# Performance work log

Measured on AMD Instinct MI355X. Metric: run time of the kernel, lower is better.

Reference implementation:

```python
import math
import jax
import jax.numpy as jnp
import numpy as np

B = 2; Hrv = 16; Wrv = 1024; Crv = 64; Cb = 128; Cout = 128
D = 128; K = 5; NH = 8; NP = 4; DH = D // NH
Hbev = 220; Wbev = 220
RMAX = 55.0; XMIN = -55.0; XMAX = 55.0; YMIN = -55.0; YMAX = 55.0
EDGE_GAIN = 4.0; KLW = 1e-4

ELEV = np.array([-30.67, -29.33, -28.0, -26.66, -25.33, -24.0, -22.67, -21.33, -20.0, -18.67, -17.33, -16.0, -14.67, -13.33, -12.0, -10.67, -9.33, -8.0, -6.66, -5.33, -4.0, -2.67, -1.33, 0.0, 1.33, 2.67, 4.0, 5.33, 6.67, 8.0, 9.33, 10.67], dtype=np.float32)


def _buffers():
    groups = ELEV[::-1].reshape(Hrv, 32 // Hrv)
    steps = np.deg2rad(groups.max(1) - groups.min(1)).astype(np.float32)
    # torch Tensor.repeat == tile (faithful to original, even though rows end up interleaved)
    elev_steps = np.tile(steps, Wrv).reshape(Hrv, Wrv)
    means = np.deg2rad(groups.mean(1)).astype(np.float32)
    elevation = np.repeat(means, Wrv).reshape(Hrv, Wrv)  # numpy repeat == elementwise
    az_line = np.linspace(-np.pi, np.pi, Wrv + 1, dtype=np.float64)[:-1]
    az_step = float(az_line[1] - az_line[0])
    az_line = (az_line + az_step / 2).astype(np.float32)
    azimuth = np.broadcast_to(az_line[None, :], (Hrv, Wrv)).astype(np.float32).copy()
    offsets = np.linspace(-0.6, 0.6, K).astype(np.float32)
    u_vec = np.stack([np.cos(elevation) * np.cos(azimuth), np.cos(elevation) * np.sin(azimuth), np.sin(elevation)], 0).astype(np.float32)
    return (jnp.asarray(elev_steps), jnp.asarray(elevation), jnp.asarray(azimuth), az_step, jnp.asarray(offsets), jnp.asarray(u_vec))


def conv1x1(x, w, b):
    return jnp.einsum('bchw,oc->bohw', x, w) + b[None, :, None, None]


def groupnorm(x, g, gamma, beta, eps=1e-5):
    b_, c, h, w = x.shape
    xr = x.reshape(b_, g, c // g, h, w)
    m = xr.mean(axis=(2, 3, 4), keepdims=True)
    v = xr.var(axis=(2, 3, 4), keepdims=True)
    xn = ((xr - m) * jax.lax.rsqrt(v + eps)).reshape(b_, c, h, w)
    return xn * gamma[None, :, None, None] + beta[None, :, None, None]


def bilinear_sample(v_t, loc, H, W):
    # v_t: [B,NH,H*W,DH]; loc: [B,Nq,NH,NP,2] in [0,1]; grid_sample align_corners=False, zeros pad
    x = loc[..., 0] * W - 0.5
    y = loc[..., 1] * H - 0.5
    x0 = jnp.floor(x); y0 = jnp.floor(y)
    wx = x - x0; wy = y - y0
    x0i = x0.astype(jnp.int32); y0i = y0.astype(jnp.int32)
    b_, n_, nh_, p_ = x.shape

    def gather(xi, yi):
        valid = (xi >= 0) & (xi < W) & (yi >= 0) & (yi < H)
        idx = jnp.clip(yi, 0, H - 1) * W + jnp.clip(xi, 0, W - 1)
        idx_t = idx.transpose(0, 2, 1, 3).reshape(b_, nh_, n_ * p_)
        g = jnp.take_along_axis(v_t, idx_t[..., None], axis=2).reshape(b_, nh_, n_, p_, -1)
        return g * valid.transpose(0, 2, 1, 3)[..., None]

    wxt = wx.transpose(0, 2, 1, 3)[..., None]
    wyt = wy.transpose(0, 2, 1, 3)[..., None]
    g = gather(x0i, y0i) * (1 - wxt) * (1 - wyt)
    g = g + gather(x0i + 1, y0i) * wxt * (1 - wyt)
    g = g + gather(x0i, y0i + 1) * (1 - wxt) * wyt
    g = g + gather(x0i + 1, y0i + 1) * wxt * wyt
    return g  # [B,NH,Nq,NP,DH]


def setup_inputs():
    key = jax.random.key(0)
    ks = jax.random.split(key, 20)
    def rn(k, shape, s=0.02):
        return jax.random.normal(k, shape, jnp.float32) * s
    inp = {}
    inp['x_rv'] = jax.random.normal(ks[0], (B, Hrv, Wrv, Crv), jnp.float32)
    inp['bev'] = jax.random.normal(ks[1], (B, Cb, Hbev, Wbev), jnp.float32)
    inp['lidar2ego_mat'] = jnp.eye(4, dtype=jnp.float32)[None] + 0.01 * jax.random.normal(ks[2], (1, 4, 4), jnp.float32)
    inp['w_q'] = rn(ks[3], (D, Crv)); inp['b_q'] = jnp.zeros((D,), jnp.float32)
    inp['w_v'] = rn(ks[4], (D, Cb)); inp['b_v'] = jnp.zeros((D,), jnp.float32)
    inp['w_o'] = rn(ks[5], (Cout, D)); inp['b_o'] = jnp.zeros((Cout,), jnp.float32)
    inp['qs_w1'] = rn(ks[6], (D, D + 6)); inp['qs_b1'] = jnp.zeros((D,), jnp.float32)
    inp['qs_w2'] = rn(ks[7], (D, D)); inp['qs_b2'] = jnp.zeros((D,), jnp.float32)
    inp['rh_w1'] = rn(ks[8], (128, Crv + 3)); inp['rh_b1'] = jnp.zeros((128,), jnp.float32)
    inp['rh_g1'] = jnp.ones((128,), jnp.float32); inp['rh_bt1'] = jnp.zeros((128,), jnp.float32)
    inp['rh_w2'] = rn(ks[9], (64, 128, 3, 3))
    inp['rh_g2'] = jnp.ones((64,), jnp.float32); inp['rh_bt2'] = jnp.zeros((64,), jnp.float32)
    inp['rh_w3'] = rn(ks[10], (4, 64)); inp['rh_b3'] = jnp.zeros((4,), jnp.float32)
    inp['off_w'] = rn(ks[11], (NH * K * NP * 2, D)); inp['off_b'] = rn(ks[12], (NH * K * NP * 2,), 0.5)
    inp['aw_w'] = rn(ks[13], (NH * K * NP, D)); inp['aw_b'] = jnp.zeros((NH * K * NP,), jnp.float32)
    inp['val_w'] = rn(ks[14], (D, D)); inp['val_b'] = jnp.zeros((D,), jnp.float32)
    inp['out_w'] = rn(ks[15], (D, D)); inp['out_b'] = jnp.zeros((D,), jnp.float32)
    return inp


def reference(x_rv, bev, lidar2ego_mat, w_q, b_q, w_v, b_v, w_o, b_o, qs_w1, qs_b1, qs_w2, qs_b2, rh_w1, rh_b1, rh_g1, rh_bt1, rh_w2, rh_g2, rh_bt2, rh_w3, rh_b3, off_w, off_b, aw_w, aw_b, val_w, val_b, out_w, out_b):
    elev_steps, elevation, azimuth, az_step, offsets, u_vec = _buffers()
    x = jnp.transpose(x_rv, (0, 3, 1, 2))  # [B,Crv,Hrv,Wrv]
    Q0 = conv1x1(x, w_q, b_q)
    Vmap = conv1x1(bev, w_v, b_v)
    range_in = jnp.concatenate([x, jnp.broadcast_to(u_vec[None], (B, 3, Hrv, Wrv))], axis=1)
    h = jax.nn.gelu(groupnorm(conv1x1(range_in, rh_w1, rh_b1), 8, rh_g1, rh_bt1), approximate=False)
    hp = jnp.pad(h, ((0, 0), (0, 0), (1, 1), (1, 1)), mode='wrap')  # circular padding
    h = jax.lax.conv_general_dilated(hp, rh_w2, (1, 1), 'VALID', dimension_numbers=('NCHW', 'OIHW', 'NCHW'))
    h = jax.nn.gelu(groupnorm(h, 8, rh_g2, rh_bt2), approximate=False)
    head = conv1x1(h, rh_w3, rh_b3)  # [B,4,Hrv,Wrv]
    mu = jax.nn.sigmoid(head[:, 0:1]) * RMAX
    sd = jax.nn.softplus(head[:, 1:2]) + 1e-3
    se = jax.nn.sigmoid(head[:, 2:3]) * elev_steps + 1e-3
    sa = jax.nn.sigmoid(head[:, 3:4]) * az_step + 1e-3
    depth = mu[:, 0][..., None] + sd[:, 0][..., None] * offsets  # [B,Hrv,Wrv,K]
    elevs = elevation[None, :, :, None] + se[:, 0][..., None] * offsets
    azs = azimuth[None, :, :, None] + sa[:, 0][..., None] * offsets
    ce = jnp.cos(elevs)
    x_l = depth * ce * jnp.cos(azs)
    y_l = depth * ce * jnp.sin(azs)
    z_l = depth * jnp.sin(elevs)
    NK = Hrv * Wrv * K
    p = jnp.stack([x_l.reshape(B, NK), y_l.reshape(B, NK), z_l.reshape(B, NK), jnp.ones((B, NK), x_l.dtype)], axis=-1)
    p_ego = jnp.matmul(p, lidar2ego_mat)  # [B,NK,4]
    rx = jax.nn.sigmoid(EDGE_GAIN * ((p_ego[..., 0] - XMIN) / (XMAX - XMIN) - 0.5))
    ry = jax.nn.sigmoid(EDGE_GAIN * ((p_ego[..., 1] - YMIN) / (YMAX - YMIN) - 0.5))
    ref = jnp.stack([rx, ry], axis=-1).reshape(B, Hrv * Wrv, K, 2)
    sig_feat = jnp.concatenate([sd, se, sa, 1.0 / (sd + 1e-6), 1.0 / (se + 1e-6), 1.0 / (sa + 1e-6)], axis=1)
    Q = conv1x1(jax.nn.gelu(conv1x1(jnp.concatenate([Q0, sig_feat], axis=1), qs_w1, qs_b1), approximate=False), qs_w2, qs_b2)
    query = jnp.transpose(Q, (0, 2, 3, 1)).reshape(B, Hrv * Wrv, D)
    value = jnp.transpose(Vmap.reshape(B, D, Hbev * Wbev), (0, 2, 1))  # [B,HW,D]
    # MSDA -- all K levels share the same BEV value map (value was repeat(1,K,1))
    v = (value @ val_w.T + val_b).reshape(B, Hbev * Wbev, NH, DH)
    v_t = jnp.transpose(v, (0, 2, 1, 3))  # [B,NH,HW,DH]
    Nq = Hrv * Wrv
    smp_off = (query @ off_w.T + off_b).reshape(B, Nq, NH, K, NP, 2)
    attn = jax.nn.softmax((query @ aw_w.T + aw_b).reshape(B, Nq, NH, K * NP), axis=-1).reshape(B, Nq, NH, K, NP)
    norm = jnp.array([Wbev, Hbev], jnp.float32)
    loc = ref[:, :, None, :, None, :] + smp_off / norm  # [B,Nq,NH,K,NP,2]
    out = jnp.zeros((B, Nq, NH, DH), jnp.float32)
    for l in range(K):
        smp = bilinear_sample(v_t, loc[:, :, :, l], Hbev, Wbev)
        out = out + jnp.einsum('bhnpd,bnhp->bnhd', smp, attn[:, :, :, l])
    y_msda = out.reshape(B, Nq, D) @ out_w.T + out_b + query  # mmcv identity residual
    y = jnp.transpose(y_msda.reshape(B, Hrv, Wrv, D), (0, 3, 1, 2))
    y = conv1x1(y, w_o, b_o)
    mu_norm = mu / RMAX
    sr = jnp.maximum(sd, 1e-6)
    saz = sa / az_step
    sel = se / elev_steps
    L_kl = 0.5 * (mu_norm ** 2 + sr ** 2 - jnp.log(sr ** 2) - 1.0) \
         + 0.5 * (saz ** 2 - jnp.log(saz ** 2) - 1.0) \
         + 0.5 * (sel ** 2 - jnp.log(sel ** 2) - 1.0)
    kl = KLW * L_kl.mean()
    y = y.reshape(B, Hrv, Wrv, -1)  # faithful to torch .view on NCHW (no permute)
    return (y, kl)
```

## Files before the change

### kernel.cpp

```cpp
#include <hip/hip_runtime.h>
#include <math.h>

#define HRV 16
#define WRV 1024
#define NPIX 16384
#define NBEV 48400
#define BSZ 2

typedef __attribute__((ext_vector_type(8))) short short8;
typedef __attribute__((ext_vector_type(4))) float f32x4;

struct RVConsts {
  float steps[16];
  float means[16];
  float az_step_f;
  float pad_;
  double step_d;
  double az0;
  double az_half;
};

__device__ __forceinline__ float geluf(float x) {
  return 0.5f * x * (1.0f + erff(x * 0.70710678118654752440f));
}
__device__ __forceinline__ float sigmoidf_(float x) {
  return 1.0f / (1.0f + expf(-x));
}
__device__ __forceinline__ float softplusf_(float x) {
  return fmaxf(x, 0.0f) + log1pf(expf(-fabsf(x)));
}
__device__ __forceinline__ float azimf(int w, double step_d, double az0, double az_half) {
  double az = (double)w * step_d + az0;
  az += az_half;
  return (float)az;
}
__device__ __forceinline__ unsigned short f2bf(float f) {
  unsigned int u = __builtin_bit_cast(unsigned int, f);
  u = u + 0x7FFFu + ((u >> 16) & 1u);
  return (unsigned short)(u >> 16);
}
__device__ __forceinline__ float bf2f(unsigned short h) {
  unsigned int u = ((unsigned int)h) << 16;
  return __builtin_bit_cast(float, u);
}

__global__ __launch_bounds__(256) void k_rh1_q0(
    const float* __restrict__ x_rv,
    const unsigned short* __restrict__ rhW1p, const float* __restrict__ rh_b1,
    const unsigned short* __restrict__ wqp, const float* __restrict__ b_q,
    float* __restrict__ t1, unsigned short* __restrict__ q0,
    float* __restrict__ sums1, RVConsts C) {
  __shared__ unsigned short xin[64][104];
  __shared__ float wred[4][8][2];
  int b = blockIdx.y;
  int n0 = blockIdx.x * 64;
  int tid = threadIdx.x;
  const float* src = x_rv + ((size_t)b * NPIX + n0) * 64;
  for (int i = tid; i < 1024; i += 256) {
    int p = i >> 4, c = (i & 15) * 4;
    float4 v4 = *(const float4*)(src + p * 64 + c);
    xin[p][c] = f2bf(v4.x);
    xin[p][c + 1] = f2bf(v4.y);
    xin[p][c + 2] = f2bf(v4.z);
    xin[p][c + 3] = f2bf(v4.w);
  }
  if (tid < 64) {
    int n = n0 + tid;
    int h = n >> 10, w = n & 1023;
    float E = C.means[h];
    float A = azimf(w, C.step_d, C.az0, C.az_half);
    float ce = cosf(E);
    xin[tid][64] = f2bf(ce * cosf(A));
    xin[tid][65] = f2bf(ce * sinf(A));
    xin[tid][66] = f2bf(sinf(E));
    for (int c = 67; c < 104; c++) xin[tid][c] = 0;
  }
  __syncthreads();
  int wave = tid >> 6, l = tid & 63;
  int lr = l & 15, lk = l >> 4;
  f32x4 acc[8], accq[8];
#pragma unroll
  for (int nt = 0; nt < 8; nt++) {
    float b1 = rh_b1[nt * 16 + lr], b2 = b_q[nt * 16 + lr];
    acc[nt] = (f32x4){b1, b1, b1, b1};
    accq[nt] = (f32x4){b2, b2, b2, b2};
  }
#pragma unroll
  for (int ks = 0; ks < 3; ks++) {
    short8 a = *(const short8*)&xin[wave * 16 + lr][ks * 32 + lk * 8];
#pragma unroll
    for (int nt = 0; nt < 8; nt++) {
      short8 b1v = *(const short8*)(rhW1p + (size_t)(nt * 16 + lr) * 96 + ks * 32 + lk * 8);
      acc[nt] = __builtin_amdgcn_mfma_f32_16x16x32_bf16(a, b1v, acc[nt], 0, 0, 0);
      short8 b2v = *(const short8*)(wqp + (size_t)(nt * 16 + lr) * 96 + ks * 32 + lk * 8);
      accq[nt] = __builtin_amdgcn_mfma_f32_16x16x32_bf16(a, b2v, accq[nt], 0, 0, 0);
    }
  }
#pragma unroll
  for (int nt = 0; nt < 8; nt++) {
    int n = nt * 16 + lr;
#pragma unroll
    for (int r = 0; r < 4; r++) {
      int p = n0 + wave * 16 + lk * 4 + r;
      size_t o = ((size_t)b * NPIX + p) * 128 + n;
      t1[o] = acc[nt][r];
      q0[o] = f2bf(accq[nt][r]);
    }
  }
  float s1[8], ss1[8];
#pragma unroll
  for (int nt = 0; nt < 8; nt++) {
    float a0 = acc[nt][0], a1 = acc[nt][1], a2 = acc[nt][2], a3 = acc[nt][3];
    s1[nt] = a0 + a1 + a2 + a3;
    ss1[nt] = a0 * a0 + a1 * a1 + a2 * a2 + a3 * a3;
  }
#pragma unroll
  for (int nt = 0; nt < 8; nt++) {
    s1[nt] += __shfl_xor(s1[nt], 1);  ss1[nt] += __shfl_xor(ss1[nt], 1);
    s1[nt] += __shfl_xor(s1[nt], 2);  ss1[nt] += __shfl_xor(ss1[nt], 2);
    s1[nt] += __shfl_xor(s1[nt], 4);  ss1[nt] += __shfl_xor(ss1[nt], 4);
    s1[nt] += __shfl_xor(s1[nt], 8);  ss1[nt] += __shfl_xor(ss1[nt], 8);
    s1[nt] += __shfl_xor(s1[nt], 16); ss1[nt] += __shfl_xor(ss1[nt], 16);
    s1[nt] += __shfl_xor(s1[nt], 32); ss1[nt] += __shfl_xor(ss1[nt], 32);
  }
  if (l == 0) {
#pragma unroll
    for (int nt = 0; nt < 8; nt++) { wred[wave][nt][0] = s1[nt]; wred[wave][nt][1] = ss1[nt]; }
  }
  __syncthreads();
  if (tid < 8) {
    float S = wred[0][tid][0] + wred[1][tid][0] + wred[2][tid][0] + wred[3][tid][0];
    float SS = wred[0][tid][1] + wred[1][tid][1] + wred[2][tid][1] + wred[3][tid][1];
    sums1[(((size_t)b * 8 + tid) * 256 + blockIdx.x) * 2 + 0] = S;
    sums1[(((size_t)b * 8 + tid) * 256 + blockIdx.x) * 2 + 1] = SS;
  }
}

__device__ __forceinline__ int cswz2(int row, int colw, int c) {
  int byte = ((row * 10 + colw) << 8) + (c << 1);
  return byte ^ ((row & 7) << 4);
}
__global__ __launch_bounds__(256) void k_conv3g(
    const float* __restrict__ t1, const float* __restrict__ sums1,
    const float* __restrict__ g1, const float* __restrict__ bt1,
    const unsigned short* __restrict__ w2p,
    float* __restrict__ t2, float* __restrict__ sums2) {
  __shared__ unsigned short tile[16 * 10 * 128];
  __shared__ float st[8][2];
  __shared__ float wred[4][2][4][2];
  int b = blockIdx.y;
  int w0 = blockIdx.x * 8;
  int tid = threadIdx.x;
  if (tid < 8) {
    int g = tid;
    float S = 0.f, SS = 0.f;
    for (int ch = 0; ch < 256; ch++) {
      S += sums1[(((size_t)b * 8 + g) * 256 + ch) * 2];
      SS += sums1[(((size_t)b * 8 + g) * 256 + ch) * 2 + 1];
    }
    float m = S * (1.0f / 262144.0f);
    float var = SS * (1.0f / 262144.0f) - m * m;
    st[g][0] = m;
    st[g][1] = rsqrtf(var + 1e-5f);
  }
  __syncthreads();
  for (int i = tid; i < 5120; i += 256) {
    int row = i / 320;
    int rem = i - row * 320;
    int colw = rem >> 5;
    int c4 = (rem & 31) * 4;
    int wc = (w0 + colw - 1 + WRV) & (WRV - 1);
    float4 x4 = *(const float4*)(t1 + ((size_t)b * NPIX + row * WRV + wc) * 128 + c4);
    int g = c4 >> 4;
    float m = st[g][0], is = st[g][1];
    float4 g4 = *(const float4*)(g1 + c4);
    float4 b4 = *(const float4*)(bt1 + c4);
    float y0 = geluf((x4.x - m) * is * g4.x + b4.x);
    float y1 = geluf((x4.y - m) * is * g4.y + b4.y);
    float y2 = geluf((x4.z - m) * is * g4.z + b4.z);
    float y3 = geluf((x4.w - m) * is * g4.w + b4.w);
    uint2 o;
    o.x = (unsigned int)f2bf(y0) | ((unsigned int)f2bf(y1) << 16);
    o.y = (unsigned int)f2bf(y2) | ((unsigned int)f2bf(y3) << 16);
    *(uint2*)((char*)tile + cswz2(row, colw, c4)) = o;
  }
  __syncthreads();
  int wave = tid >> 6, l = tid & 63;
  int lr = l & 15, lk = l >> 4;
  f32x4 acc[2][4];
#pragma unroll
  for (int cc2 = 0; cc2 < 2; cc2++)
#pragma unroll
    for (int nt = 0; nt < 4; nt++) acc[cc2][nt] = (f32x4){0.f, 0.f, 0.f, 0.f};
#pragma unroll
  for (int kpos = 0; kpos < 9; kpos++) {
    int ky = kpos / 3, kx = kpos - ky * 3;
    int arow = (lr + ky - 1 + 16) & 15;
#pragma unroll
    for (int cc2 = 0; cc2 < 2; cc2++) {
      int acol = wave * 2 + cc2 + kx;
#pragma unroll
      for (int ks = 0; ks < 4; ks++) {
        short8 a = *(const short8*)((const char*)tile + cswz2(arow, acol, ks * 32 + lk * 8));
#pragma unroll
        for (int nt = 0; nt < 4; nt++) {
          short8 bv = *(const short8*)(w2p + (size_t)(kpos * 64 + nt * 16 + lr) * 128 +
                                       ks * 32 + lk * 8);
          acc[cc2][nt] = __builtin_amdgcn_mfma_f32_16x16x32_bf16(a, bv, acc[cc2][nt], 0, 0, 0);
        }
      }
    }
  }
#pragma unroll
  for (int cc2 = 0; cc2 < 2; cc2++) {
    int cc = wave * 2 + cc2;
#pragma unroll
    for (int nt = 0; nt < 4; nt++) {
      int o = nt * 16 + lr;
#pragma unroll
      for (int r = 0; r < 4; r++) {
        int p = (lk * 4 + r) * WRV + w0 + cc;
        t2[((size_t)b * NPIX + p) * 64 + o] = acc[cc2][nt][r];
      }
    }
  }
  float ps[4], pss[4];
#pragma unroll
  for (int nt = 0; nt < 4; nt++) { ps[nt] = 0.f; pss[nt] = 0.f; }
#pragma unroll
  for (int cc2 = 0; cc2 < 2; cc2++)
#pragma unroll
    for (int nt = 0; nt < 4; nt++)
#pragma unroll
      for (int r = 0; r < 4; r++) {
        float v = acc[cc2][nt][r];
        ps[nt] += v;
        pss[nt] += v * v;
      }
#pragma unroll
  for (int nt = 0; nt < 4; nt++) {
    ps[nt] += __shfl_xor(ps[nt], 1);  pss[nt] += __shfl_xor(pss[nt], 1);
    ps[nt] += __shfl_xor(ps[nt], 2);  pss[nt] += __shfl_xor(pss[nt], 2);
    ps[nt] += __shfl_xor(ps[nt], 4);  pss[nt] += __shfl_xor(pss[nt], 4);
    ps[nt] += __shfl_xor(ps[nt], 16); pss[nt] += __shfl_xor(pss[nt], 16);
    ps[nt] += __shfl_xor(ps[nt], 32); pss[nt] += __shfl_xor(pss[nt], 32);
  }
  if ((l & 0x37) == 0) {
    int b3 = (l >> 3) & 1;
#pragma unroll
    for (int nt = 0; nt < 4; nt++) {
      wred[wave][b3][nt][0] = ps[nt];
      wred[wave][b3][nt][1] = pss[nt];
    }
  }
  __syncthreads();
  if (tid < 8) {
    int nt = tid >> 1, b3 = tid & 1;
    float S = 0.f, SS = 0.f;
    for (int wv = 0; wv < 4; wv++) { S += wred[wv][b3][nt][0]; SS += wred[wv][b3][nt][1]; }
    int g = nt * 2 + b3;
    sums2[(((size_t)b * 8 + g) * 128 + blockIdx.x) * 2 + 0] = S;
    sums2[(((size_t)b * 8 + g) * 128 + blockIdx.x) * 2 + 1] = SS;
  }
}

__global__ __launch_bounds__(256) void k_headquery(
    const float* __restrict__ t2, const float* __restrict__ sums2,
    const float* __restrict__ g2, const float* __restrict__ bt2,
    const float* __restrict__ rh_w3, const float* __restrict__ rh_b3,
    const float* __restrict__ l2e, const unsigned short* __restrict__ q0,
    const unsigned short* __restrict__ qsW1p, const float* __restrict__ qs_b1,
    const float* __restrict__ qs_w1f,
    const unsigned short* __restrict__ qsW2p, const float* __restrict__ qs_b2,
    float* __restrict__ params, float* __restrict__ klpart,
    unsigned short* __restrict__ query, RVConsts C) {
  __shared__ float st2[8][2];
  __shared__ unsigned short qin[64][136];
  __shared__ unsigned short hq[64][136];
  __shared__ float sigf[64][6];
  __shared__ float klred[64];
  int b = blockIdx.y;
  int n0 = blockIdx.x * 64;
  int tid = threadIdx.x;
  if (tid < 8) {
    int g = tid;
    float S = 0.f, SS = 0.f;
    for (int ch = 0; ch < 128; ch++) {
      S += sums2[(((size_t)b * 8 + g) * 128 + ch) * 2];
      SS += sums2[(((size_t)b * 8 + g) * 128 + ch) * 2 + 1];
    }
    float m = S * (1.0f / 131072.0f);
    float var = SS * (1.0f / 131072.0f) - m * m;
    st2[g][0] = m;
    st2[g][1] = rsqrtf(var + 1e-5f);
  }
  const unsigned short* src = q0 + ((size_t)b * NPIX + n0) * 128;
  for (int i = tid; i < 1024; i += 256) {
    int p = i >> 4, c0 = (i & 15) * 8;
    *(uint4*)&qin[p][c0] = *(const uint4*)(src + p * 128 + c0);
  }
  __syncthreads();
  {
    int px = tid >> 2, q = tid & 3;
    int n = n0 + px;
    int h = n >> 10, w = n & 1023;
    const float* t = t2 + ((size_t)b * NPIX + n) * 64 + q * 16;
    float hd0 = 0.f, hd1 = 0.f, hd2 = 0.f, hd3 = 0.f;
#pragma unroll
    for (int j = 0; j < 16; j++) {
      int c = q * 16 + j;
      int g = c >> 3;
      float xv = geluf((t[j] - st2[g][0]) * st2[g][1] * g2[c] + bt2[c]);
      hd0 += rh_w3[c] * xv;
      hd1 += rh_w3[64 + c] * xv;
      hd2 += rh_w3[128 + c] * xv;
      hd3 += rh_w3[192 + c] * xv;
    }
    hd0 += __shfl_xor(hd0, 1); hd1 += __shfl_xor(hd1, 1);
    hd2 += __shfl_xor(hd2, 1); hd3 += __shfl_xor(hd3, 1);
    hd0 += __shfl_xor(hd0, 2); hd1 += __shfl_xor(hd1, 2);
    hd2 += __shfl_xor(hd2, 2); hd3 += __shfl_xor(hd3, 2);
    if (q == 0) {
      hd0 += rh_b3[0]; hd1 += rh_b3[1]; hd2 += rh_b3[2]; hd3 += rh_b3[3];
      float mu = sigmoidf_(hd0) * 55.0f;
      float sd = softplusf_(hd1) + 1e-3f;
      float stepw = C.steps[w & 15];
      float se = sigmoidf_(hd2) * stepw + 1e-3f;
      float sa = sigmoidf_(hd3) * C.az_step_f + 1e-3f;
      float E0 = C.means[h];
      float A0 = azimf(w, C.step_d, C.az0, C.az_half);
      float* P = params + ((size_t)b * NPIX + n) * 16;
      P[0] = sd; P[1] = se; P[2] = sa;
      sigf[px][0] = sd; sigf[px][1] = se; sigf[px][2] = sa;
      sigf[px][3] = 1.0f / (sd + 1e-6f);
      sigf[px][4] = 1.0f / (se + 1e-6f);
      sigf[px][5] = 1.0f / (sa + 1e-6f);
      float M00 = l2e[0], M01 = l2e[1], M10 = l2e[4], M11 = l2e[5];
      float M20 = l2e[8], M21 = l2e[9], M30 = l2e[12], M31 = l2e[13];
#pragma unroll
      for (int k = 0; k < 5; k++) {
        float off = -0.6f + 0.3f * (float)k;
        float d = mu + sd * off;
        float E = E0 + se * off;
        float A = A0 + sa * off;
        float ce = cosf(E);
        float xl = d * ce * cosf(A), yl = d * ce * sinf(A), zl = d * sinf(E);
        float px_ = xl * M00 + yl * M10 + zl * M20 + M30;
        float py_ = xl * M01 + yl * M11 + zl * M21 + M31;
        P[3 + 2 * k] = sigmoidf_(4.0f * ((px_ + 55.0f) * (1.0f / 110.0f) - 0.5f));
        P[4 + 2 * k] = sigmoidf_(4.0f * ((py_ + 55.0f) * (1.0f / 110.0f) - 0.5f));
      }
      float mu_n = mu * (1.0f / 55.0f);
      float sr = fmaxf(sd, 1e-6f);
      float saz = sa / C.az_step_f;
      float sel = se / stepw;
      klred[px] = 0.5f * (mu_n * mu_n + sr * sr - logf(sr * sr) - 1.0f) +
                  0.5f * (saz * saz - logf(saz * saz) - 1.0f) +
                  0.5f * (sel * sel - logf(sel * sel) - 1.0f);
    }
  }
  __syncthreads();
  if (tid == 0) {
    float sL = 0.f;
    for (int i = 0; i < 64; i++) sL += klred[i];
    klpart[b * 256 + blockIdx.x] = sL;
  }
  int wave = tid >> 6, l = tid & 63;
  int lr = l & 15, lk = l >> 4;
  f32x4 acc[8];
#pragma unroll
  for (int nt = 0; nt < 8; nt++) {
    int n = nt * 16 + lr;
    float wt[6];
#pragma unroll
    for (int c = 0; c < 6; c++) wt[c] = qs_w1f[(size_t)n * 134 + 128 + c];
    float bias = qs_b1[n];
#pragma unroll
    for (int r = 0; r < 4; r++) {
      int pl = wave * 16 + lk * 4 + r;
      float a = bias;
#pragma unroll
      for (int c = 0; c < 6; c++) a += wt[c] * sigf[pl][c];
      acc[nt][r] = a;
    }
  }
#pragma unroll
  for (int ks = 0; ks < 4; ks++) {
    short8 a = *(const short8*)&qin[wave * 16 + lr][ks * 32 + lk * 8];
#pragma unroll
    for (int nt = 0; nt < 8; nt++) {
      short8 bv = *(const short8*)(qsW1p + (size_t)(nt * 16 + lr) * 128 + ks * 32 + lk * 8);
      acc[nt] = __builtin_amdgcn_mfma_f32_16x16x32_bf16(a, bv, acc[nt], 0, 0, 0);
    }
  }
#pragma unroll
  for (int nt = 0; nt < 8; nt++)
#pragma unroll
    for (int r = 0; r < 4; r++)
      hq[wave * 16 + lk * 4 + r][nt * 16 + lr] = f2bf(geluf(acc[nt][r]));
  __syncthreads();
#pragma unroll
  for (int nt = 0; nt < 8; nt++) {
    float bias = qs_b2[nt * 16 + lr];
    acc[nt] = (f32x4){bias, bias, bias, bias};
  }
#pragma unroll
  for (int ks = 0; ks < 4; ks++) {
    short8 a = *(const short8*)&hq[wave * 16 + lr][ks * 32 + lk * 8];
#pragma unroll
    for (int nt = 0; nt < 8; nt++) {
      short8 bv = *(const short8*)(qsW2p + (size_t)(nt * 16 + lr) * 128 + ks * 32 + lk * 8);
      acc[nt] = __builtin_amdgcn_mfma_f32_16x16x32_bf16(a, bv, acc[nt], 0, 0, 0);
    }
  }
#pragma unroll
  for (int nt = 0; nt < 8; nt++) {
    int n = nt * 16 + lr;
#pragma unroll
    for (int r = 0; r < 4; r++) {
      int p = n0 + wave * 16 + lk * 4 + r;
      query[((size_t)b * NPIX + p) * 128 + n] = f2bf(acc[nt][r]);
    }
  }
}

__global__ __launch_bounds__(256) void k_pack(
    const float* __restrict__ val_w, const float* __restrict__ w_v,
    const float* __restrict__ b_v, const float* __restrict__ val_b,
    const float* __restrict__ off_w, const float* __restrict__ off_b,
    const float* __restrict__ aw_w, const float* __restrict__ aw_b,
    const float* __restrict__ out_w, const float* __restrict__ qs_w1,
    const float* __restrict__ qs_w2, const float* __restrict__ rh_w1,
    const float* __restrict__ w_q, const float* __restrict__ w_o,
    const float* __restrict__ rh_w2,
    unsigned short* __restrict__ wvv_bf, float* __restrict__ bvv,
    unsigned short* __restrict__ projW, float* __restrict__ projB,
    unsigned short* __restrict__ outW, unsigned short* __restrict__ qsW1p,
    unsigned short* __restrict__ qsW2p, unsigned short* __restrict__ rhW1p,
    unsigned short* __restrict__ wqp, unsigned short* __restrict__ woP,
    unsigned short* __restrict__ w2p) {
  int idx = blockIdx.x * 256 + threadIdx.x;
  if (idx < 16384) {
    int o = idx >> 7, c = idx & 127;
    float acc = 0.0f;
    for (int m = 0; m < 128; m++) acc += val_w[o * 128 + m] * w_v[m * 128 + c];
    wvv_bf[idx] = f2bf(acc);
  } else if (idx < 16512) {
    int o = idx - 16384;
    float acc = val_b[o];
    for (int m = 0; m < 128; m++) acc += val_w[o * 128 + m] * b_v[m];
    bvv[o] = acc;
  } else if (idx < 82048) {
    int j = idx - 16512;
    int r = j >> 7, c = j & 127;
    float w = (r < 320) ? off_w[r * 128 + c] : ((r < 480) ? aw_w[(r - 320) * 128 + c] : 0.0f);
    projW[j] = f2bf(w);
  } else if (idx < 82560) {
    int r = idx - 82048;
    projB[r] = (r < 320) ? off_b[r] : ((r < 480) ? aw_b[r - 320] : 0.0f);
  } else if (idx < 98944) {
    int j = idx - 82560;
    outW[j] = f2bf(out_w[j]);
  } else if (idx < 115328) {
    int j = idx - 98944;
    int r = j >> 7, c = j & 127;
    qsW1p[j] = f2bf(qs_w1[r * 134 + c]);
  } else if (idx < 131712) {
    int j = idx - 115328;
    qsW2p[j] = f2bf(qs_w2[j]);
  } else if (idx < 144000) {
    int j = idx - 131712;
    int r = j / 96, c = j - r * 96;
    rhW1p[j] = (c < 67) ? f2bf(rh_w1[r * 67 + c]) : 0;
  } else if (idx < 156288) {
    int j = idx - 144000;
    int r = j / 96, c = j - r * 96;
    wqp[j] = (c < 64) ? f2bf(w_q[r * 64 + c]) : 0;
  } else if (idx < 172672) {
    int j = idx - 156288;
    woP[j] = f2bf(w_o[j]);
  } else if (idx < 246400) {
    int j = idx - 172672;
    int kpos = j >> 13;
    int rem = j & 8191;
    int o = rem >> 7, c = rem & 127;
    int ky = kpos / 3, kx = kpos - ky * 3;
    w2p[j] = f2bf(rh_w2[((size_t)(o * 128 + c) * 3 + ky) * 3 + kx]);
  }
}

__global__ __launch_bounds__(256) void k_value(
    const float* __restrict__ bev, const unsigned short* __restrict__ wvv_bf,
    const float* __restrict__ bvv, unsigned short* __restrict__ v) {
  __shared__ float lds[128 * 66];
  int b = blockIdx.y;
  int p0 = blockIdx.x * 64;
  int tid = threadIdx.x;
  int npx = NBEV - p0; if (npx > 64) npx = 64;
  for (int i = tid; i < 128 * 64; i += 256) {
    int c = i >> 6, p = i & 63;
    lds[c * 66 + p] = (p < npx) ? bev[((size_t)b * 128 + c) * NBEV + p0 + p] : 0.0f;
  }
  __syncthreads();
  int wave = tid >> 6, l = tid & 63;
  int lr = l & 15, lk = l >> 4;
  int ploc = wave * 16 + lr;
  f32x4 acc[8];
#pragma unroll
  for (int nt = 0; nt < 8; nt++) {
    float bias = bvv[nt * 16 + lr];
    acc[nt] = (f32x4){bias, bias, bias, bias};
  }
#pragma unroll
  for (int ks = 0; ks < 4; ks++) {
    int k0 = ks * 32 + lk * 8;
    short8 a;
#pragma unroll
    for (int j = 0; j < 8; j++) a[j] = (short)f2bf(lds[(k0 + j) * 66 + ploc]);
#pragma unroll
    for (int nt = 0; nt < 8; nt++) {
      short8 bf = *(const short8*)(wvv_bf + (size_t)(nt * 16 + lr) * 128 + k0);
      acc[nt] = __builtin_amdgcn_mfma_f32_16x16x32_bf16(a, bf, acc[nt], 0, 0, 0);
    }
  }
#pragma unroll
  for (int nt = 0; nt < 8; nt++) {
    int n = nt * 16 + lr;
#pragma unroll
    for (int r = 0; r < 4; r++) {
      int p = p0 + wave * 16 + lk * 4 + r;
      if (p < NBEV) v[((size_t)b * NBEV + p) * 128 + n] = f2bf(acc[nt][r]);
    }
  }
}

__global__ __launch_bounds__(256) void k_proj(
    const unsigned short* __restrict__ query, const unsigned short* __restrict__ projW,
    const float* __restrict__ projB, unsigned short* __restrict__ proj) {
  __shared__ unsigned short qlds[64][136];
  int b = blockIdx.y;
  int p0b = blockIdx.x * 64;
  int tid = threadIdx.x;
  const unsigned short* src = query + ((size_t)b * NPIX + p0b) * 128;
  for (int i = tid; i < 1024; i += 256) {
    int p = i >> 4, c0 = (i & 15) * 8;
    *(uint4*)&qlds[p][c0] = *(const uint4*)(src + p * 128 + c0);
  }
  __syncthreads();
  int wave = tid >> 6, l = tid & 63;
  int lr = l & 15, lk = l >> 4;
  int p0 = p0b + wave * 16;
  for (int nc = 0; nc < 4; nc++) {
    int n0 = nc * 128;
    f32x4 acc[8];
#pragma unroll
    for (int nt = 0; nt < 8; nt++) {
      float bias = projB[n0 + nt * 16 + lr];
      acc[nt] = (f32x4){bias, bias, bias, bias};
    }
#pragma unroll
    for (int ks = 0; ks < 4; ks++) {
      short8 a = *(const short8*)&qlds[wave * 16 + lr][ks * 32 + lk * 8];
#pragma unroll
      for (int nt = 0; nt < 8; nt++) {
        short8 bf = *(const short8*)(projW + (size_t)(n0 + nt * 16 + lr) * 128 +
                                     ks * 32 + lk * 8);
        acc[nt] = __builtin_amdgcn_mfma_f32_16x16x32_bf16(a, bf, acc[nt], 0, 0, 0);
      }
    }
#pragma unroll
    for (int nt = 0; nt < 8; nt++) {
      int n = n0 + nt * 16 + lr;
#pragma unroll
      for (int r = 0; r < 4; r++) {
        int p = p0 + lk * 4 + r;
        proj[((size_t)b * NPIX + p) * 512 + n] = f2bf(acc[nt][r]);
      }
    }
  }
}

__global__ __launch_bounds__(256) void k_samp(
    const unsigned short* __restrict__ proj, const float* __restrict__ params,
    const unsigned short* __restrict__ v, unsigned short* __restrict__ S) {
  int b = blockIdx.y;
  int bid = blockIdx.x;
  int pb = (bid & 7) * 256 + (bid >> 3);
  int tid = threadIdx.x;
  int q = tid & 3, hh = (tid >> 2) & 7, pl = tid >> 5;
  int n = pb * 8 + pl;
  const unsigned short* base = proj + ((size_t)b * NPIX + n) * 512;
  float lg[5];
#pragma unroll
  for (int t = 0; t < 5; t++) lg[t] = bf2f(base[320 + hh * 20 + q * 5 + t]);
  float mx = fmaxf(fmaxf(fmaxf(lg[0], lg[1]), fmaxf(lg[2], lg[3])), lg[4]);
  mx = fmaxf(mx, __shfl_xor(mx, 1));
  mx = fmaxf(mx, __shfl_xor(mx, 2));
  float e[5];
  float s = 0.0f;
#pragma unroll
  for (int t = 0; t < 5; t++) { e[t] = expf(lg[t] - mx); s += e[t]; }
  s += __shfl_xor(s, 1);
  s += __shfl_xor(s, 2);
  float rs = 1.0f / s;
  const float* P = params + ((size_t)b * NPIX + n) * 16;
  const unsigned short* vb = v + (size_t)b * NBEV * 128 + hh * 16;
  float acc[16];
#pragma unroll
  for (int c = 0; c < 16; c++) acc[c] = 0.0f;
#pragma unroll
  for (int t = 0; t < 5; t++) {
    int kp = q * 5 + t;
    int k = kp >> 2;
    unsigned int u = *(const unsigned int*)(base + hh * 40 + kp * 2);
    float X = P[3 + 2 * k] * 220.0f - 0.5f + bf2f((unsigned short)(u & 0xffffu));
    float Y = P[4 + 2 * k] * 220.0f - 0.5f + bf2f((unsigned short)(u >> 16));
    float xf = floorf(X), yf = floorf(Y);
    float wx = X - xf, wy = Y - yf;
    int x0 = (int)xf, y0 = (int)yf;
    float wx0 = ((unsigned)x0 < 220u) ? (1.0f - wx) : 0.0f;
    float wx1 = ((unsigned)(x0 + 1) < 220u) ? wx : 0.0f;
    float wy0 = ((unsigned)y0 < 220u) ? (1.0f - wy) : 0.0f;
    float wy1 = ((unsigned)(y0 + 1) < 220u) ? wy : 0.0f;
    int cx0 = min(max(x0, 0), 219), cx1 = min(max(x0 + 1, 0), 219);
    int cy0 = min(max(y0, 0), 219) * 220, cy1 = min(max(y0 + 1, 0), 219) * 220;
    float a = e[t] * rs;
    float u0 = a * wy0, u1 = a * wy1;
    float w4[4] = {u0 * wx0, u0 * wx1, u1 * wx0, u1 * wx1};
    int i4[4] = {cy0 + cx0, cy0 + cx1, cy1 + cx0, cy1 + cx1};
#pragma unroll
    for (int c2 = 0; c2 < 4; c2++) {
      float w = w4[c2];
      const uint4* sp = (const uint4*)(vb + (size_t)i4[c2] * 128);
      uint4 r0 = sp[0], r1 = sp[1];
      acc[0] += w * bf2f((unsigned short)(r0.x & 0xffffu));
      acc[1] += w * bf2f((unsigned short)(r0.x >> 16));
      acc[2] += w * bf2f((unsigned short)(r0.y & 0xffffu));
      acc[3] += w * bf2f((unsigned short)(r0.y >> 16));
      acc[4] += w * bf2f((unsigned short)(r0.z & 0xffffu));
      acc[5] += w * bf2f((unsigned short)(r0.z >> 16));
      acc[6] += w * bf2f((unsigned short)(r0.w & 0xffffu));
      acc[7] += w * bf2f((unsigned short)(r0.w >> 16));
      acc[8] += w * bf2f((unsigned short)(r1.x & 0xffffu));
      acc[9] += w * bf2f((unsigned short)(r1.x >> 16));
      acc[10] += w * bf2f((unsigned short)(r1.y & 0xffffu));
      acc[11] += w * bf2f((unsigned short)(r1.y >> 16));
      acc[12] += w * bf2f((unsigned short)(r1.z & 0xffffu));
      acc[13] += w * bf2f((unsigned short)(r1.z >> 16));
      acc[14] += w * bf2f((unsigned short)(r1.w & 0xffffu));
      acc[15] += w * bf2f((unsigned short)(r1.w >> 16));
    }
  }
#pragma unroll
  for (int c = 0; c < 16; c++) {
    acc[c] += __shfl_xor(acc[c], 1);
    acc[c] += __shfl_xor(acc[c], 2);
  }
  if (q == 0) {
    uint4 o1, o2;
    o1.x = (unsigned int)f2bf(acc[0]) | ((unsigned int)f2bf(acc[1]) << 16);
    o1.y = (unsigned int)f2bf(acc[2]) | ((unsigned int)f2bf(acc[3]) << 16);
    o1.z = (unsigned int)f2bf(acc[4]) | ((unsigned int)f2bf(acc[5]) << 16);
    o1.w = (unsigned int)f2bf(acc[6]) | ((unsigned int)f2bf(acc[7]) << 16);
    o2.x = (unsigned int)f2bf(acc[8]) | ((unsigned int)f2bf(acc[9]) << 16);
    o2.y = (unsigned int)f2bf(acc[10]) | ((unsigned int)f2bf(acc[11]) << 16);
    o2.z = (unsigned int)f2bf(acc[12]) | ((unsigned int)f2bf(acc[13]) << 16);
    o2.w = (unsigned int)f2bf(acc[14]) | ((unsigned int)f2bf(acc[15]) << 16);
    unsigned short* dst = S + ((size_t)b * NPIX + n) * 128 + hh * 16;
    *(uint4*)dst = o1;
    *(uint4*)(dst + 8) = o2;
  }
}

__global__ __launch_bounds__(256) void k_outfinal(
    const unsigned short* __restrict__ S, const unsigned short* __restrict__ outW,
    const float* __restrict__ out_b, const unsigned short* __restrict__ query,
    const unsigned short* __restrict__ woP, const float* __restrict__ b_o,
    const float* __restrict__ klpart, float* __restrict__ out) {
  __shared__ unsigned short ylds[64][136];
  __shared__ float yt[128][67];
  int b = blockIdx.y;
  int p0b = blockIdx.x * 64;
  int tid = threadIdx.x;
  int wave = tid >> 6, l = tid & 63;
  int lr = l & 15, lk = l >> 4;
  {
    f32x4 acc[8];
#pragma unroll
    for (int nt = 0; nt < 8; nt++) {
      float bias = out_b[nt * 16 + lr];
      acc[nt] = (f32x4){bias, bias, bias, bias};
    }
    const unsigned short* ap = S + ((size_t)b * NPIX + p0b + wave * 16 + lr) * 128 + lk * 8;
#pragma unroll
    for (int ks = 0; ks < 4; ks++) {
      short8 a = *(const short8*)(ap + ks * 32);
#pragma unroll
      for (int nt = 0; nt < 8; nt++) {
        short8 bf = *(const short8*)(outW + (size_t)(nt * 16 + lr) * 128 + ks * 32 + lk * 8);
        acc[nt] = __builtin_amdgcn_mfma_f32_16x16x32_bf16(a, bf, acc[nt], 0, 0, 0);
      }
    }
#pragma unroll
    for (int nt = 0; nt < 8; nt++) {
      int n = nt * 16 + lr;
#pragma unroll
      for (int r = 0; r < 4; r++) {
        int p_local = wave * 16 + lk * 4 + r;
        size_t o = ((size_t)b * NPIX + p0b + p_local) * 128 + n;
        ylds[p_local][n] = f2bf(acc[nt][r] + bf2f(query[o]));
      }
    }
  }
  __syncthreads();
  {
    f32x4 acc[8];
#pragma unroll
    for (int nt = 0; nt < 8; nt++) {
      float bias = b_o[nt * 16 + lr];
      acc[nt] = (f32x4){bias, bias, bias, bias};
    }
#pragma unroll
    for (int ks = 0; ks < 4; ks++) {
      short8 a = *(const short8*)&ylds[wave * 16 + lr][ks * 32 + lk * 8];
#pragma unroll
      for (int nt = 0; nt < 8; nt++) {
        short8 bf = *(const short8*)(woP + (size_t)(nt * 16 + lr) * 128 + ks * 32 + lk * 8);
        acc[nt] = __builtin_amdgcn_mfma_f32_16x16x32_bf16(a, bf, acc[nt], 0, 0, 0);
      }
    }
#pragma unroll
    for (int nt = 0; nt < 8; nt++)
#pragma unroll
      for (int r = 0; r < 4; r++)
        yt[nt * 16 + lr][wave * 16 + lk * 4 + r] = acc[nt][r];
  }
  __syncthreads();
  int n = tid >> 1, half = tid & 1;
  float* dst = out + ((size_t)(b * 128 + n)) * NPIX + p0b + half * 32;
#pragma unroll
  for (int j = 0; j < 8; j++) {
    float4 v4 = {yt[n][half * 32 + j * 4], yt[n][half * 32 + j * 4 + 1],
                 yt[n][half * 32 + j * 4 + 2], yt[n][half * 32 + j * 4 + 3]};
    *(float4*)(dst + j * 4) = v4;
  }
  if (blockIdx.x == 0 && b == 0 && tid == 0) {
    float sL = 0.0f;
    for (int i = 0; i < 512; i++) sL += klpart[i];
    out[(size_t)BSZ * 128 * NPIX] = 1e-4f * (sL / 32768.0f);
  }
}

static RVConsts make_consts() {
  static const float ELEV[32] = {
      -30.67f, -29.33f, -28.0f, -26.66f, -25.33f, -24.0f, -22.67f, -21.33f,
      -20.0f,  -18.67f, -17.33f, -16.0f, -14.67f, -13.33f, -12.0f, -10.67f,
      -9.33f,  -8.0f,   -6.66f,  -5.33f, -4.0f,   -2.67f,  -1.33f, 0.0f,
      1.33f,   2.67f,   4.0f,    5.33f,  6.67f,   8.0f,    9.33f,  10.67f};
  RVConsts C;
  const float d2r = 0.017453292519943295f;
  for (int r = 0; r < 16; r++) {
    float a = ELEV[31 - 2 * r], b = ELEV[30 - 2 * r];
    float mx = fmaxf(a, b), mn = fminf(a, b);
    C.steps[r] = (mx - mn) * d2r;
    C.means[r] = ((a + b) * 0.5f) * d2r;
  }
  const double PI_D = 3.14159265358979323846;
  double step_d = (PI_D - (-PI_D)) / 1024.0;
  double az0 = -PI_D;
  double az1 = az0 + step_d;
  double az_step_d = az1 - az0;
  C.az_step_f = (float)az_step_d;
  C.pad_ = 0.0f;
  C.step_d = step_d;
  C.az0 = az0;
  C.az_half = az_step_d * 0.5;
  return C;
}

#define OFF_T1     0u
#define OFF_T2     8388608u
#define OFF_Q0     10485760u
#define OFF_PARAMS 14680064u
#define OFF_QUERY  15204352u
#define OFF_S      19398656u
#define OFF_SUMS1  21495808u
#define OFF_SUMS2  21504000u
#define OFF_KL     21508096u
#define OFF_PROJ   0u
#define OFF_V      8388608u
#define OFF_WVV    21508608u
#define OFF_BVV    21516800u
#define OFF_PROJW  21516928u
#define OFF_PROJB  21549696u
#define OFF_OUTW   21550208u
#define OFF_QSW1   21558400u
#define OFF_QSW2   21566592u
#define OFF_RHW1   21574784u
#define OFF_WQP    21580928u
#define OFF_WOP    21587072u
#define OFF_W2P    21595264u

extern "C" void kernel_launch(void* const* d_in, const int* in_sizes, int n_in,
                              void* d_out, int out_size, void* d_ws, size_t ws_size,
                              hipStream_t stream) {
  const float* x_rv = (const float*)d_in[0];
  const float* bev = (const float*)d_in[1];
  const float* l2e = (const float*)d_in[2];
  const float* w_q = (const float*)d_in[3];
  const float* b_q = (const float*)d_in[4];
  const float* w_v = (const float*)d_in[5];
  const float* b_v = (const float*)d_in[6];
  const float* w_o = (const float*)d_in[7];
  const float* b_o = (const float*)d_in[8];
  const float* qs_w1 = (const float*)d_in[9];
  const float* qs_b1 = (const float*)d_in[10];
  const float* qs_w2 = (const float*)d_in[11];
  const float* qs_b2 = (const float*)d_in[12];
  const float* rh_w1 = (const float*)d_in[13];
  const float* rh_b1 = (const float*)d_in[14];
  const float* rh_g1 = (const float*)d_in[15];
  const float* rh_bt1 = (const float*)d_in[16];
  const float* rh_w2 = (const float*)d_in[17];
  const float* rh_g2 = (const float*)d_in[18];
  const float* rh_bt2 = (const float*)d_in[19];
  const float* rh_w3 = (const float*)d_in[20];
  const float* rh_b3 = (const float*)d_in[21];
  const float* off_w = (const float*)d_in[22];
  const float* off_b = (const float*)d_in[23];
  const float* aw_w = (const float*)d_in[24];
  const float* aw_b = (const float*)d_in[25];
  const float* val_w = (const float*)d_in[26];
  const float* val_b = (const float*)d_in[27];
  const float* out_w = (const float*)d_in[28];
  const float* out_b = (const float*)d_in[29];

  float* ws = (float*)d_ws;
  float* t1 = ws + OFF_T1;
  float* t2 = ws + OFF_T2;
  float* params = ws + OFF_PARAMS;
  float* sums1 = ws + OFF_SUMS1;
  float* sums2 = ws + OFF_SUMS2;
  float* klpart = ws + OFF_KL;
  float* bvv = ws + OFF_BVV;
  float* projB = ws + OFF_PROJB;
  unsigned short* q0bf = (unsigned short*)(ws + OFF_Q0);
  unsigned short* querybf = (unsigned short*)(ws + OFF_QUERY);
  unsigned short* S_bf = (unsigned short*)(ws + OFF_S);
  unsigned short* proj_bf = (unsigned short*)(ws + OFF_PROJ);
  unsigned short* v_bf = (unsigned short*)(ws + OFF_V);
  unsigned short* wvv_bf = (unsigned short*)(ws + OFF_WVV);
  unsigned short* projW = (unsigned short*)(ws + OFF_PROJW);
  unsigned short* outW = (unsigned short*)(ws + OFF_OUTW);
  unsigned short* qsW1p = (unsigned short*)(ws + OFF_QSW1);
  unsigned short* qsW2p = (unsigned short*)(ws + OFF_QSW2);
  unsigned short* rhW1p = (unsigned short*)(ws + OFF_RHW1);
  unsigned short* wqp = (unsigned short*)(ws + OFF_WQP);
  unsigned short* woP = (unsigned short*)(ws + OFF_WOP);
  unsigned short* w2p = (unsigned short*)(ws + OFF_W2P);

  RVConsts C = make_consts();
  dim3 blk(256);

  k_pack<<<963, blk, 0, stream>>>(val_w, w_v, b_v, val_b, off_w, off_b, aw_w, aw_b, out_w,
                                  qs_w1, qs_w2, rh_w1, w_q, w_o, rh_w2,
                                  wvv_bf, bvv, projW, projB, outW, qsW1p, qsW2p, rhW1p,
                                  wqp, woP, w2p);
  k_rh1_q0<<<dim3(256, BSZ), blk, 0, stream>>>(x_rv, rhW1p, rh_b1, wqp, b_q, t1, q0bf,
                                               sums1, C);
  k_conv3g<<<dim3(128, BSZ), blk, 0, stream>>>(t1, sums1, rh_g1, rh_bt1, w2p, t2, sums2);
  k_headquery<<<dim3(256, BSZ), blk, 0, stream>>>(t2, sums2, rh_g2, rh_bt2, rh_w3, rh_b3,
                                                  l2e, q0bf, qsW1p, qs_b1, qs_w1, qsW2p,
                                                  qs_b2, params, klpart, querybf, C);
  k_value<<<dim3(757, BSZ), blk, 0, stream>>>(bev, wvv_bf, bvv, v_bf);
  k_proj<<<dim3(256, BSZ), blk, 0, stream>>>(querybf, projW, projB, proj_bf);
  k_samp<<<dim3(2048, BSZ), blk, 0, stream>>>(proj_bf, params, v_bf, S_bf);
  k_outfinal<<<dim3(256, BSZ), blk, 0, stream>>>(S_bf, outW, out_b, querybf, woP, b_o,
                                                 klpart, (float*)d_out);
}
```

Measured before the change: 294.2 us.

## Split per-head channels across two threads in the sampling kernel

The deformable-attention sampling kernel now gives each head's 16 channels to two threads of 8 channels each. Threads per query point double, so the grid grows from 2048 to 4096 blocks, and each thread holds half as many accumulators and issues half-width 8-byte gathers. The aim is more memory-level parallelism and lower register pressure for the latency-bound bilinear gathers. The cost is that every thread pair now repeats the softmax, offset and bilinear-weight arithmetic, and the kernel issues more, smaller load instructions.

```diff
diff --git a/kernel.cpp b/kernel.cpp
--- a/kernel.cpp
+++ b/kernel.cpp
@@ -585,32 +585,35 @@
     const unsigned short* __restrict__ v, unsigned short* __restrict__ S) {
   int b = blockIdx.y;
   int bid = blockIdx.x;
-  int pb = (bid & 7) * 256 + (bid >> 3);
+  int pb = (bid & 7) * 512 + (bid >> 3);
   int tid = threadIdx.x;
-  int q = tid & 3, hh = (tid >> 2) & 7, pl = tid >> 5;
-  int n = pb * 8 + pl;
+  int g = tid & 7;
+  int hh = (tid >> 3) & 7;
+  int pl = tid >> 6;
+  int ts = g >> 1, th = g & 1;
+  int n = pb * 4 + pl;
   const unsigned short* base = proj + ((size_t)b * NPIX + n) * 512;
   float lg[5];
 #pragma unroll
-  for (int t = 0; t < 5; t++) lg[t] = bf2f(base[320 + hh * 20 + q * 5 + t]);
+  for (int t = 0; t < 5; t++) lg[t] = bf2f(base[320 + hh * 20 + ts * 5 + t]);
   float mx = fmaxf(fmaxf(fmaxf(lg[0], lg[1]), fmaxf(lg[2], lg[3])), lg[4]);
-  mx = fmaxf(mx, __shfl_xor(mx, 1));
   mx = fmaxf(mx, __shfl_xor(mx, 2));
+  mx = fmaxf(mx, __shfl_xor(mx, 4));
   float e[5];
   float s = 0.0f;
 #pragma unroll
   for (int t = 0; t < 5; t++) { e[t] = expf(lg[t] - mx); s += e[t]; }
-  s += __shfl_xor(s, 1);
   s += __shfl_xor(s, 2);
+  s += __shfl_xor(s, 4);
   float rs = 1.0f / s;
   const float* P = params + ((size_t)b * NPIX + n) * 16;
-  const unsigned short* vb = v + (size_t)b * NBEV * 128 + hh * 16;
-  float acc[16];
-#pragma unroll
-  for (int c = 0; c < 16; c++) acc[c] = 0.0f;
+  const unsigned short* vb = v + (size_t)b * NBEV * 128 + hh * 16 + th * 8;
+  float acc[8];
+#pragma unroll
+  for (int c = 0; c < 8; c++) acc[c] = 0.0f;
 #pragma unroll
   for (int t = 0; t < 5; t++) {
-    int kp = q * 5 + t;
+    int kp = ts * 5 + t;
     int k = kp >> 2;
     unsigned int u = *(const unsigned int*)(base + hh * 40 + kp * 2);
     float X = P[3 + 2 * k] * 220.0f - 0.5f + bf2f((unsigned short)(u & 0xffffu));
@@ -631,44 +634,30 @@
 #pragma unroll
     for (int c2 = 0; c2 < 4; c2++) {
       float w = w4[c2];
-      const uint4* sp = (const uint4*)(vb + (size_t)i4[c2] * 128);
-      uint4 r0 = sp[0], r1 = sp[1];
+      const uint2* sp = (const uint2*)(vb + (size_t)i4[c2] * 128);
+      uint2 r0 = sp[0], r1 = sp[1];
       acc[0] += w * bf2f((unsigned short)(r0.x & 0xffffu));
       acc[1] += w * bf2f((unsigned short)(r0.x >> 16));
       acc[2] += w * bf2f((unsigned short)(r0.y & 0xffffu));
       acc[3] += w * bf2f((unsigned short)(r0.y >> 16));
-      acc[4] += w * bf2f((unsigned short)(r0.z & 0xffffu));
-      acc[5] += w * bf2f((unsigned short)(r0.z >> 16));
-      acc[6] += w * bf2f((unsigned short)(r0.w & 0xffffu));
-      acc[7] += w * bf2f((unsigned short)(r0.w >> 16));
-      acc[8] += w * bf2f((unsigned short)(r1.x & 0xffffu));
-      acc[9] += w * bf2f((unsigned short)(r1.x >> 16));
-      acc[10] += w * bf2f((unsigned short)(r1.y & 0xffffu));
-      acc[11] += w * bf2f((unsigned short)(r1.y >> 16));
-      acc[12] += w * bf2f((unsigned short)(r1.z & 0xffffu));
-      acc[13] += w * bf2f((unsigned short)(r1.z >> 16));
-      acc[14] += w * bf2f((unsigned short)(r1.w & 0xffffu));
-      acc[15] += w * bf2f((unsigned short)(r1.w >> 16));
-    }
-  }
-#pragma unroll
-  for (int c = 0; c < 16; c++) {
-    acc[c] += __shfl_xor(acc[c], 1);
+      acc[4] += w * bf2f((unsigned short)(r1.x & 0xffffu));
+      acc[5] += w * bf2f((unsigned short)(r1.x >> 16));
+      acc[6] += w * bf2f((unsigned short)(r1.y & 0xffffu));
+      acc[7] += w * bf2f((unsigned short)(r1.y >> 16));
+    }
+  }
+#pragma unroll
+  for (int c = 0; c < 8; c++) {
     acc[c] += __shfl_xor(acc[c], 2);
-  }
-  if (q == 0) {
-    uint4 o1, o2;
+    acc[c] += __shfl_xor(acc[c], 4);
+  }
+  if (ts == 0) {
+    uint4 o1;
     o1.x = (unsigned int)f2bf(acc[0]) | ((unsigned int)f2bf(acc[1]) << 16);
     o1.y = (unsigned int)f2bf(acc[2]) | ((unsigned int)f2bf(acc[3]) << 16);
     o1.z = (unsigned int)f2bf(acc[4]) | ((unsigned int)f2bf(acc[5]) << 16);
     o1.w = (unsigned int)f2bf(acc[6]) | ((unsigned int)f2bf(acc[7]) << 16);
-    o2.x = (unsigned int)f2bf(acc[8]) | ((unsigned int)f2bf(acc[9]) << 16);
-    o2.y = (unsigned int)f2bf(acc[10]) | ((unsigned int)f2bf(acc[11]) << 16);
-    o2.z = (unsigned int)f2bf(acc[12]) | ((unsigned int)f2bf(acc[13]) << 16);
-    o2.w = (unsigned int)f2bf(acc[14]) | ((unsigned int)f2bf(acc[15]) << 16);
-    unsigned short* dst = S + ((size_t)b * NPIX + n) * 128 + hh * 16;
-    *(uint4*)dst = o1;
-    *(uint4*)(dst + 8) = o2;
+    *(uint4*)(S + ((size_t)b * NPIX + n) * 128 + hh * 16 + th * 8) = o1;
   }
 }
 
@@ -874,7 +863,7 @@
                                                   qs_b2, params, klpart, querybf, C);
   k_value<<<dim3(757, BSZ), blk, 0, stream>>>(bev, wvv_bf, bvv, v_bf);
   k_proj<<<dim3(256, BSZ), blk, 0, stream>>>(querybf, projW, projB, proj_bf);
-  k_samp<<<dim3(2048, BSZ), blk, 0, stream>>>(proj_bf, params, v_bf, S_bf);
+  k_samp<<<dim3(4096, BSZ), blk, 0, stream>>>(proj_bf, params, v_bf, S_bf);
   k_outfinal<<<dim3(256, BSZ), blk, 0, stream>>>(S_bf, outW, out_b, querybf, woP, b_o,
                                                  klpart, (float*)d_out);
 }
```

Measured after the change: 277.0 us. 1.06x faster.
